# Optimization experiments

Measured on AMD Instinct MI355X. Metric: run time of the kernel, lower is better.

## Reference

```python
import jax, jax.numpy as jnp
import numpy as np

LN_EPS = 1e-5

def _layernorm(x, scale, bias):
    mu = jnp.mean(x, axis=-1, keepdims=True)
    var = jnp.var(x, axis=-1, keepdims=True)
    return (x - mu) * jax.lax.rsqrt(var + LN_EPS) * scale + bias

def setup_inputs() -> dict:
    T, node_num, num_nodes, E, C = 4, 10000, 50000, 256, 128
    key = jax.random.key(0)
    ks = jax.random.split(key, 12)
    s = lambda fan_in: 1.0 / np.sqrt(fan_in)
    return {
        "x": jax.random.normal(ks[0], (T * node_num, E), jnp.float32),
        "batched_x": jax.random.normal(ks[1], (num_nodes, E), jnp.float32),
        "indices": jax.random.randint(ks[2], (T, node_num), 0, num_nodes, jnp.int32),
        "ln_d_scale": jnp.ones((E,), jnp.float32),
        "ln_d_bias": jnp.zeros((E,), jnp.float32),
        "W1_d": jax.random.normal(ks[3], (E, 2 * E), jnp.float32) * s(E),
        "b1_d": jnp.zeros((2 * E,), jnp.float32),
        "W2_d": jax.random.normal(ks[4], (2 * E, C), jnp.float32) * s(2 * E),
        "b2_d": jnp.zeros((C,), jnp.float32),
        "ln_u_scale": jnp.ones((C,), jnp.float32),
        "ln_u_bias": jnp.zeros((C,), jnp.float32),
        "W1_u": jax.random.normal(ks[5], (C, 2 * C), jnp.float32) * s(C),
        "b1_u": jnp.zeros((2 * C,), jnp.float32),
        "W2_u": jax.random.normal(ks[6], (2 * C, E), jnp.float32) * s(2 * C),
        "b2_u": jnp.zeros((E,), jnp.float32),
    }

def reference(x, batched_x, indices, ln_d_scale, ln_d_bias, W1_d, b1_d, W2_d, b2_d,
              ln_u_scale, ln_u_bias, W1_u, b1_u, W2_u, b2_u):
    T, node_num = indices.shape
    num_nodes, E = batched_x.shape
    xr = x.reshape(T, node_num, E)
    # _to_entire: per-step scatter-add of active-node embeddings into the full node table
    def scatter_one(xi, idx):
        return jnp.zeros((num_nodes, E), x.dtype).at[idx].add(xi)
    ta = jax.vmap(scatter_one)(xr, indices)          # [T, num_nodes, E]
    inp = ta + batched_x[None]                        # broadcast entire features
    h = _layernorm(inp, ln_d_scale, ln_d_bias)
    h = jax.nn.gelu(h @ W1_d + b1_d, approximate=False) @ W2_d + b2_d  # [T, num_nodes, C]
    # _from_entire: gather each step's active nodes back, concat, LN + MLP up
    g = jnp.take_along_axis(h, indices[..., None], axis=1)  # [T, node_num, C]
    g = g.reshape(T * node_num, -1)
    g = _layernorm(g, ln_u_scale, ln_u_bias)
    out = jax.nn.gelu(g @ W1_u + b1_u, approximate=False) @ W2_u + b2_u  # [T*node_num, E]
    return out
```

## Files before the change

kernel.cpp:

```cpp
#include <hip/hip_runtime.h>
#include <math.h>

#define T_STEPS   4
#define NODE_NUM  10000
#define NUM_NODES 50000
#define E         256
#define TWO_E     512
#define CC        128
#define TWO_C     256
#define ROWS      32

typedef short bf16x8 __attribute__((ext_vector_type(8)));
typedef float f32x4  __attribute__((ext_vector_type(4)));

#define MFMA16(a, b, c) __builtin_amdgcn_mfma_f32_16x16x32_bf16((a), (b), (c), 0, 0, 0)

static __device__ unsigned short g_wt[294912];
static __device__ int g_cnt[T_STEPS * NUM_NODES];

__device__ __forceinline__ float geluf(float v) {
    return 0.5f * v * (1.0f + erff(v * 0.70710678118654752440f));
}

__device__ __forceinline__ unsigned short f2bf(float f) {
    unsigned int u = __builtin_bit_cast(unsigned int, f);
    u += 0x7fffu + ((u >> 16) & 1u);
    return (unsigned short)(u >> 16);
}

__global__ void prep_weights(const float* __restrict__ W1d, const float* __restrict__ W2d,
                             const float* __restrict__ W1u, const float* __restrict__ W2u) {
    int i = blockIdx.x * 256 + threadIdx.x;
    if (i < T_STEPS * NUM_NODES) g_cnt[i] = 0;
    if (i < 131072) {
        int n = i >> 8, k = i & 255;
        g_wt[i] = f2bf(W1d[(size_t)k * TWO_E + n]);
    }
    if (i < 65536) {
        int n = i >> 9, k = i & 511;
        g_wt[131072 + i] = f2bf(W2d[(size_t)k * CC + n]);
    }
    if (i < 32768) {
        int n = i >> 7, k = i & 127;
        g_wt[196608 + i] = f2bf(W1u[(size_t)k * TWO_C + n]);
    }
    if (i < 65536) {
        int n = i >> 8, k = i & 255;
        g_wt[229376 + i] = f2bf(W2u[(size_t)k * E + n]);
    }
}

__global__ void count_kernel(const int* __restrict__ indices) {
    int gr = blockIdx.x * 256 + threadIdx.x;
    if (gr < T_STEPS * NODE_NUM) {
        int t = gr / NODE_NUM;
        atomicAdd(&g_cnt[t * NUM_NODES + indices[gr]], 1);
    }
}

__global__ void zero_dup_kernel(float* __restrict__ table,
                                const int* __restrict__ indices,
                                int gr0, int t0) {
    int gr = gr0 + blockIdx.x * 4 + (threadIdx.x >> 6);
    int t = gr / NODE_NUM;
    int idx = indices[gr];
    if (g_cnt[t * NUM_NODES + idx] < 2) return;
    int c = (threadIdx.x & 63) * 4;
    float4 z = make_float4(0.f, 0.f, 0.f, 0.f);
    *reinterpret_cast<float4*>(&table[((size_t)(t - t0) * NUM_NODES + idx) * E + c]) = z;
}

__global__ void scatter_dup_kernel(float* __restrict__ table,
                                   const float* __restrict__ x,
                                   const int* __restrict__ indices,
                                   int gr0, int t0) {
    int gr = gr0 + blockIdx.x;
    int t = gr / NODE_NUM;
    int idx = indices[gr];
    if (g_cnt[t * NUM_NODES + idx] < 2) return;
    atomicAdd(&table[((size_t)(t - t0) * NUM_NODES + idx) * E + threadIdx.x],
              x[(size_t)gr * E + threadIdx.x]);
}

__global__ __launch_bounds__(256, 3)
void mlp_kernel(const float* __restrict__ table,
                const float* __restrict__ x,
                const float* __restrict__ batched_x,
                const int* __restrict__ indices,
                const float* __restrict__ lnd_s, const float* __restrict__ lnd_b,
                const float* __restrict__ b1d, const float* __restrict__ b2d,
                const float* __restrict__ lnu_s, const float* __restrict__ lnu_b,
                const float* __restrict__ b1u, const float* __restrict__ b2u,
                float* __restrict__ out,
                int gr0, int t0, int grLim) {
    __shared__ __align__(16) unsigned char smem[50176];
    __shared__ const float* rptr[ROWS];
    __shared__ int    ridx[ROWS];

    float*          Xf  = (float*)smem;
    unsigned short* Xs  = (unsigned short*)(smem + 33280);
    unsigned short* H1  = (unsigned short*)smem;
    float*          H2f = (float*)(smem + 33280);
    unsigned short* H2b = (unsigned short*)smem;
    unsigned short* G1  = (unsigned short*)(smem + 8704);

    const unsigned short* w1t  = g_wt;
    const unsigned short* w2t  = g_wt + 131072;
    const unsigned short* w1ut = g_wt + 196608;
    const unsigned short* w2ut = g_wt + 229376;

    const int tid = threadIdx.x;
    const int w = tid >> 6, lane = tid & 63;
    const int l16 = lane & 15, quad = lane >> 4;
    const int grb = gr0 + blockIdx.x * ROWS;

    if (tid < ROWS) {
        int gr = grb + tid;
        if (gr >= grLim) gr = grLim - 1;
        int t = gr / NODE_NUM;
        int idx = indices[gr];
        ridx[tid] = idx;
        rptr[tid] = (g_cnt[t * NUM_NODES + idx] > 1)
            ? (table + ((size_t)(t - t0) * NUM_NODES + idx) * E)
            : (x + (size_t)gr * E);
    }
    __syncthreads();

    #pragma unroll
    for (int it = 0; it < 8; ++it) {
        int v = it * 256 + tid;
        int r = v >> 6;
        int c = (v & 63) * 4;
        float4 tv = *reinterpret_cast<const float4*>(rptr[r] + c);
        float4 bv = *reinterpret_cast<const float4*>(&batched_x[(size_t)ridx[r] * E + c]);
        float4 s; s.x = tv.x + bv.x; s.y = tv.y + bv.y; s.z = tv.z + bv.z; s.w = tv.w + bv.w;
        *reinterpret_cast<float4*>(&Xf[r * 260 + c]) = s;
    }
    __syncthreads();

    {
        int row = tid >> 3, l8 = tid & 7;
        float s = 0.f, sq = 0.f;
        #pragma unroll
        for (int k = 0; k < 32; ++k) {
            float v = Xf[row * 260 + k * 8 + l8];
            s += v; sq += v * v;
        }
        s  += __shfl_xor(s, 1);  s  += __shfl_xor(s, 2);  s  += __shfl_xor(s, 4);
        sq += __shfl_xor(sq, 1); sq += __shfl_xor(sq, 2); sq += __shfl_xor(sq, 4);
        float mu = s * (1.0f / E);
        float var = sq * (1.0f / E) - mu * mu;
        float rs = rsqrtf(var + 1e-5f);
        #pragma unroll
        for (int k = 0; k < 32; ++k) {
            int c = k * 8 + l8;
            float v = (Xf[row * 260 + c] - mu) * rs * lnd_s[c] + lnd_b[c];
            Xs[row * 264 + c] = f2bf(v);
        }
    }
    __syncthreads();

    {
        bf16x8 af[2][8];
        #pragma unroll
        for (int mt = 0; mt < 2; ++mt) {
            const unsigned short* base = Xs + (l16 + 16 * mt) * 264 + quad * 8;
            #pragma unroll
            for (int ks = 0; ks < 8; ++ks)
                af[mt][ks] = *reinterpret_cast<const bf16x8*>(base + ks * 32);
        }
        #pragma unroll
        for (int nt_ = 0; nt_ < 8; ++nt_) {
            int n = (w * 8 + nt_) * 16 + l16;
            const unsigned short* bp = w1t + (size_t)n * 256 + quad * 8;
            f32x4 a0 = {0.f, 0.f, 0.f, 0.f}, a1 = {0.f, 0.f, 0.f, 0.f};
            #pragma unroll
            for (int ks = 0; ks < 8; ++ks) {
                bf16x8 b = *reinterpret_cast<const bf16x8*>(bp + ks * 32);
                a0 = MFMA16(af[0][ks], b, a0);
                a1 = MFMA16(af[1][ks], b, a1);
            }
            float bias = b1d[n];
            #pragma unroll
            for (int reg = 0; reg < 4; ++reg) {
                int r = quad * 4 + reg;
                H1[r * 520 + n]        = f2bf(geluf(a0[reg] + bias));
                H1[(r + 16) * 520 + n] = f2bf(geluf(a1[reg] + bias));
            }
        }
    }
    __syncthreads();

    {
        f32x4 acc2[2][2];
        #pragma unroll
        for (int i = 0; i < 2; ++i)
            #pragma unroll
            for (int j = 0; j < 2; ++j) acc2[i][j] = (f32x4){0.f, 0.f, 0.f, 0.f};
        #pragma unroll
        for (int kh = 0; kh < 2; ++kh) {
            bf16x8 af2[2][8];
            #pragma unroll
            for (int mt = 0; mt < 2; ++mt) {
                const unsigned short* base = H1 + (l16 + 16 * mt) * 520 + kh * 256 + quad * 8;
                #pragma unroll
                for (int ks = 0; ks < 8; ++ks)
                    af2[mt][ks] = *reinterpret_cast<const bf16x8*>(base + ks * 32);
            }
            #pragma unroll
            for (int nt2 = 0; nt2 < 2; ++nt2) {
                int n = (w * 2 + nt2) * 16 + l16;
                const unsigned short* bp = w2t + (size_t)n * 512 + kh * 256 + quad * 8;
                #pragma unroll
                for (int ks = 0; ks < 8; ++ks) {
                    bf16x8 b = *reinterpret_cast<const bf16x8*>(bp + ks * 32);
                    acc2[nt2][0] = MFMA16(af2[0][ks], b, acc2[nt2][0]);
                    acc2[nt2][1] = MFMA16(af2[1][ks], b, acc2[nt2][1]);
                }
            }
        }
        #pragma unroll
        for (int nt2 = 0; nt2 < 2; ++nt2) {
            int n = (w * 2 + nt2) * 16 + l16;
            float bias = b2d[n];
            #pragma unroll
            for (int mt = 0; mt < 2; ++mt)
                #pragma unroll
                for (int reg = 0; reg < 4; ++reg) {
                    int r = mt * 16 + quad * 4 + reg;
                    H2f[r * 132 + n] = acc2[nt2][mt][reg] + bias;
                }
        }
    }
    __syncthreads();

    {
        int row = tid >> 3, l8 = tid & 7;
        float s = 0.f, sq = 0.f;
        #pragma unroll
        for (int k = 0; k < 16; ++k) {
            float v = H2f[row * 132 + k * 8 + l8];
            s += v; sq += v * v;
        }
        s  += __shfl_xor(s, 1);  s  += __shfl_xor(s, 2);  s  += __shfl_xor(s, 4);
        sq += __shfl_xor(sq, 1); sq += __shfl_xor(sq, 2); sq += __shfl_xor(sq, 4);
        float mu = s * (1.0f / CC);
        float var = sq * (1.0f / CC) - mu * mu;
        float rs = rsqrtf(var + 1e-5f);
        #pragma unroll
        for (int k = 0; k < 16; ++k) {
            int c = k * 8 + l8;
            float v = (H2f[row * 132 + c] - mu) * rs * lnu_s[c] + lnu_b[c];
            H2b[row * 136 + c] = f2bf(v);
        }
    }
    __syncthreads();

    {
        bf16x8 af3[2][4];
        #pragma unroll
        for (int mt = 0; mt < 2; ++mt) {
            const unsigned short* base = H2b + (l16 + 16 * mt) * 136 + quad * 8;
            #pragma unroll
            for (int ks = 0; ks < 4; ++ks)
                af3[mt][ks] = *reinterpret_cast<const bf16x8*>(base + ks * 32);
        }
        #pragma unroll
        for (int nt_ = 0; nt_ < 4; ++nt_) {
            int n = (w * 4 + nt_) * 16 + l16;
            const unsigned short* bp = w1ut + (size_t)n * 128 + quad * 8;
            f32x4 a0 = {0.f, 0.f, 0.f, 0.f}, a1 = {0.f, 0.f, 0.f, 0.f};
            #pragma unroll
            for (int ks = 0; ks < 4; ++ks) {
                bf16x8 b = *reinterpret_cast<const bf16x8*>(bp + ks * 32);
                a0 = MFMA16(af3[0][ks], b, a0);
                a1 = MFMA16(af3[1][ks], b, a1);
            }
            float bias = b1u[n];
            #pragma unroll
            for (int reg = 0; reg < 4; ++reg) {
                int r = quad * 4 + reg;
                G1[r * 264 + n]        = f2bf(geluf(a0[reg] + bias));
                G1[(r + 16) * 264 + n] = f2bf(geluf(a1[reg] + bias));
            }
        }
    }
    __syncthreads();

    {
        bf16x8 af4[2][8];
        #pragma unroll
        for (int mt = 0; mt < 2; ++mt) {
            const unsigned short* base = G1 + (l16 + 16 * mt) * 264 + quad * 8;
            #pragma unroll
            for (int ks = 0; ks < 8; ++ks)
                af4[mt][ks] = *reinterpret_cast<const bf16x8*>(base + ks * 32);
        }
        #pragma unroll
        for (int nt_ = 0; nt_ < 4; ++nt_) {
            int n = (w * 4 + nt_) * 16 + l16;
            const unsigned short* bp = w2ut + (size_t)n * 256 + quad * 8;
            f32x4 a0 = {0.f, 0.f, 0.f, 0.f}, a1 = {0.f, 0.f, 0.f, 0.f};
            #pragma unroll
            for (int ks = 0; ks < 8; ++ks) {
                bf16x8 b = *reinterpret_cast<const bf16x8*>(bp + ks * 32);
                a0 = MFMA16(af4[0][ks], b, a0);
                a1 = MFMA16(af4[1][ks], b, a1);
            }
            float bias = b2u[n];
            #pragma unroll
            for (int reg = 0; reg < 4; ++reg) {
                int r = quad * 4 + reg;
                int g0 = grb + r, g1 = grb + r + 16;
                if (g0 < grLim) out[(size_t)g0 * E + n] = a0[reg] + bias;
                if (g1 < grLim) out[(size_t)g1 * E + n] = a1[reg] + bias;
            }
        }
    }
}

extern "C" void kernel_launch(void* const* d_in, const int* in_sizes, int n_in,
                              void* d_out, int out_size, void* d_ws, size_t ws_size,
                              hipStream_t stream) {
    const float* x     = (const float*)d_in[0];
    const float* bx    = (const float*)d_in[1];
    const int*   idxp  = (const int*)  d_in[2];
    const float* lnd_s = (const float*)d_in[3];
    const float* lnd_b = (const float*)d_in[4];
    const float* W1d   = (const float*)d_in[5];
    const float* b1d   = (const float*)d_in[6];
    const float* W2d   = (const float*)d_in[7];
    const float* b2d   = (const float*)d_in[8];
    const float* lnu_s = (const float*)d_in[9];
    const float* lnu_b = (const float*)d_in[10];
    const float* W1u   = (const float*)d_in[11];
    const float* b1u   = (const float*)d_in[12];
    const float* W2u   = (const float*)d_in[13];
    const float* b2u   = (const float*)d_in[14];
    float* out = (float*)d_out;
    float* table = (float*)d_ws;

    const size_t slice_bytes = (size_t)NUM_NODES * E * sizeof(float);
    int tb = (int)(ws_size / slice_bytes);
    if (tb < 1) tb = 1;
    if (tb > T_STEPS) tb = T_STEPS;

    prep_weights<<<784, 256, 0, stream>>>(W1d, W2d, W1u, W2u);
    count_kernel<<<(T_STEPS * NODE_NUM + 255) / 256, 256, 0, stream>>>(idxp);

    for (int t0 = 0; t0 < T_STEPS; t0 += tb) {
        int tcur = T_STEPS - t0 < tb ? T_STEPS - t0 : tb;
        int nrows = tcur * NODE_NUM;
        int gr0 = t0 * NODE_NUM;
        int grLim = gr0 + nrows;
        zero_dup_kernel   <<<nrows / 4, 256, 0, stream>>>(table, idxp, gr0, t0);
        scatter_dup_kernel<<<nrows, E, 0, stream>>>(table, x, idxp, gr0, t0);
        mlp_kernel<<<(nrows + ROWS - 1) / ROWS, 256, 0, stream>>>(
            table, x, bx, idxp, lnd_s, lnd_b, b1d, b2d,
            lnu_s, lnu_b, b1u, b2u, out, gr0, t0, grLim);
    }
}
```

Before: 293.0 us.

## Compact duplicate rows and shrink MLP shared memory for higher occupancy

The duplicate-row scatter is rebuilt around a compacted list. A compaction kernel zeroes each duplicate's table row and appends its index with an atomic counter, and a grid-stride kernel then scatters only the listed rows instead of launching one block per row. In the MLP kernel, the fp32 staging buffer in LDS is removed: rows are loaded straight into registers for the layernorm, and the buffers are aliased more tightly with extra barriers, cutting LDS from about 50KB to 33KB and raising launch bounds to 4 blocks per CU. The costs are higher register pressure, extra syncs, and atomic-ordering nondeterminism in the duplicate list.

```diff
diff --git a/kernel.cpp b/kernel.cpp
--- a/kernel.cpp
+++ b/kernel.cpp
@@ -12,11 +12,14 @@
 
 typedef short bf16x8 __attribute__((ext_vector_type(8)));
 typedef float f32x4  __attribute__((ext_vector_type(4)));
+typedef unsigned short u16x4 __attribute__((ext_vector_type(4)));
 
 #define MFMA16(a, b, c) __builtin_amdgcn_mfma_f32_16x16x32_bf16((a), (b), (c), 0, 0, 0)
 
 static __device__ unsigned short g_wt[294912];
 static __device__ int g_cnt[T_STEPS * NUM_NODES];
+static __device__ int g_dup[T_STEPS * NODE_NUM];
+static __device__ int g_ndup[T_STEPS];
 
 __device__ __forceinline__ float geluf(float v) {
     return 0.5f * v * (1.0f + erff(v * 0.70710678118654752440f));
@@ -32,6 +35,7 @@
                              const float* __restrict__ W1u, const float* __restrict__ W2u) {
     int i = blockIdx.x * 256 + threadIdx.x;
     if (i < T_STEPS * NUM_NODES) g_cnt[i] = 0;
+    if (i < T_STEPS) g_ndup[i] = 0;
     if (i < 131072) {
         int n = i >> 8, k = i & 255;
         g_wt[i] = f2bf(W1d[(size_t)k * TWO_E + n]);
@@ -58,31 +62,37 @@
     }
 }
 
-__global__ void zero_dup_kernel(float* __restrict__ table,
-                                const int* __restrict__ indices,
-                                int gr0, int t0) {
-    int gr = gr0 + blockIdx.x * 4 + (threadIdx.x >> 6);
+__global__ void compact_zero_kernel(float* __restrict__ table,
+                                    const int* __restrict__ indices,
+                                    int gr0, int t0, int grLim, int slab) {
+    int gr = gr0 + blockIdx.x * 256 + threadIdx.x;
+    if (gr >= grLim) return;
     int t = gr / NODE_NUM;
     int idx = indices[gr];
     if (g_cnt[t * NUM_NODES + idx] < 2) return;
-    int c = (threadIdx.x & 63) * 4;
+    int pos = atomicAdd(&g_ndup[slab], 1);
+    g_dup[gr0 + pos] = gr;
+    float4* rp = reinterpret_cast<float4*>(&table[((size_t)(t - t0) * NUM_NODES + idx) * E]);
     float4 z = make_float4(0.f, 0.f, 0.f, 0.f);
-    *reinterpret_cast<float4*>(&table[((size_t)(t - t0) * NUM_NODES + idx) * E + c]) = z;
-}
-
-__global__ void scatter_dup_kernel(float* __restrict__ table,
-                                   const float* __restrict__ x,
-                                   const int* __restrict__ indices,
-                                   int gr0, int t0) {
-    int gr = gr0 + blockIdx.x;
-    int t = gr / NODE_NUM;
-    int idx = indices[gr];
-    if (g_cnt[t * NUM_NODES + idx] < 2) return;
-    atomicAdd(&table[((size_t)(t - t0) * NUM_NODES + idx) * E + threadIdx.x],
-              x[(size_t)gr * E + threadIdx.x]);
-}
-
-__global__ __launch_bounds__(256, 3)
+    #pragma unroll
+    for (int k = 0; k < 64; ++k) rp[k] = z;
+}
+
+__global__ void scatter_list_kernel(float* __restrict__ table,
+                                    const float* __restrict__ x,
+                                    const int* __restrict__ indices,
+                                    int gr0, int t0, int slab) {
+    int nd = g_ndup[slab];
+    for (int e = blockIdx.x; e < nd; e += gridDim.x) {
+        int gr = g_dup[gr0 + e];
+        int t = gr / NODE_NUM;
+        int idx = indices[gr];
+        atomicAdd(&table[((size_t)(t - t0) * NUM_NODES + idx) * E + threadIdx.x],
+                  x[(size_t)gr * E + threadIdx.x]);
+    }
+}
+
+__global__ __launch_bounds__(256, 4)
 void mlp_kernel(const float* __restrict__ table,
                 const float* __restrict__ x,
                 const float* __restrict__ batched_x,
@@ -93,16 +103,13 @@
                 const float* __restrict__ b1u, const float* __restrict__ b2u,
                 float* __restrict__ out,
                 int gr0, int t0, int grLim) {
-    __shared__ __align__(16) unsigned char smem[50176];
-    __shared__ const float* rptr[ROWS];
-    __shared__ int    ridx[ROWS];
-
-    float*          Xf  = (float*)smem;
-    unsigned short* Xs  = (unsigned short*)(smem + 33280);
+    __shared__ __align__(16) unsigned char smem[33280];
+
+    unsigned short* Xs  = (unsigned short*)smem;
     unsigned short* H1  = (unsigned short*)smem;
-    float*          H2f = (float*)(smem + 33280);
-    unsigned short* H2b = (unsigned short*)smem;
-    unsigned short* G1  = (unsigned short*)(smem + 8704);
+    float*          H2f = (float*)smem;
+    unsigned short* H2b = (unsigned short*)(smem + 16896);
+    unsigned short* G1  = (unsigned short*)smem;
 
     const unsigned short* w1t  = g_wt;
     const unsigned short* w2t  = g_wt + 131072;
@@ -114,48 +121,44 @@
     const int l16 = lane & 15, quad = lane >> 4;
     const int grb = gr0 + blockIdx.x * ROWS;
 
-    if (tid < ROWS) {
-        int gr = grb + tid;
+    {
+        const int row = tid >> 3, l8 = tid & 7;
+        int gr = grb + row;
         if (gr >= grLim) gr = grLim - 1;
-        int t = gr / NODE_NUM;
-        int idx = indices[gr];
-        ridx[tid] = idx;
-        rptr[tid] = (g_cnt[t * NUM_NODES + idx] > 1)
+        const int t = gr / NODE_NUM;
+        const int idx = indices[gr];
+        const float* src = (g_cnt[t * NUM_NODES + idx] > 1)
             ? (table + ((size_t)(t - t0) * NUM_NODES + idx) * E)
             : (x + (size_t)gr * E);
-    }
-    __syncthreads();
-
-    #pragma unroll
-    for (int it = 0; it < 8; ++it) {
-        int v = it * 256 + tid;
-        int r = v >> 6;
-        int c = (v & 63) * 4;
-        float4 tv = *reinterpret_cast<const float4*>(rptr[r] + c);
-        float4 bv = *reinterpret_cast<const float4*>(&batched_x[(size_t)ridx[r] * E + c]);
-        float4 s; s.x = tv.x + bv.x; s.y = tv.y + bv.y; s.z = tv.z + bv.z; s.w = tv.w + bv.w;
-        *reinterpret_cast<float4*>(&Xf[r * 260 + c]) = s;
-    }
-    __syncthreads();
-
-    {
-        int row = tid >> 3, l8 = tid & 7;
+        const float* bxp = batched_x + (size_t)idx * E;
+        float v[32];
         float s = 0.f, sq = 0.f;
         #pragma unroll
-        for (int k = 0; k < 32; ++k) {
-            float v = Xf[row * 260 + k * 8 + l8];
-            s += v; sq += v * v;
+        for (int k = 0; k < 8; ++k) {
+            const int c = k * 32 + l8 * 4;
+            float4 a = *reinterpret_cast<const float4*>(src + c);
+            float4 b = *reinterpret_cast<const float4*>(bxp + c);
+            float4 u;
+            u.x = a.x + b.x; u.y = a.y + b.y; u.z = a.z + b.z; u.w = a.w + b.w;
+            v[k*4+0] = u.x; v[k*4+1] = u.y; v[k*4+2] = u.z; v[k*4+3] = u.w;
+            s  += u.x + u.y + u.z + u.w;
+            sq += u.x*u.x + u.y*u.y + u.z*u.z + u.w*u.w;
         }
         s  += __shfl_xor(s, 1);  s  += __shfl_xor(s, 2);  s  += __shfl_xor(s, 4);
         sq += __shfl_xor(sq, 1); sq += __shfl_xor(sq, 2); sq += __shfl_xor(sq, 4);
-        float mu = s * (1.0f / E);
-        float var = sq * (1.0f / E) - mu * mu;
-        float rs = rsqrtf(var + 1e-5f);
-        #pragma unroll
-        for (int k = 0; k < 32; ++k) {
-            int c = k * 8 + l8;
-            float v = (Xf[row * 260 + c] - mu) * rs * lnd_s[c] + lnd_b[c];
-            Xs[row * 264 + c] = f2bf(v);
+        const float mu = s * (1.0f / E);
+        const float rs = rsqrtf(sq * (1.0f / E) - mu * mu + 1e-5f);
+        #pragma unroll
+        for (int k = 0; k < 8; ++k) {
+            const int c = k * 32 + l8 * 4;
+            float4 sc = *reinterpret_cast<const float4*>(lnd_s + c);
+            float4 bi = *reinterpret_cast<const float4*>(lnd_b + c);
+            u16x4 o;
+            o.x = f2bf((v[k*4+0] - mu) * rs * sc.x + bi.x);
+            o.y = f2bf((v[k*4+1] - mu) * rs * sc.y + bi.y);
+            o.z = f2bf((v[k*4+2] - mu) * rs * sc.z + bi.z);
+            o.w = f2bf((v[k*4+3] - mu) * rs * sc.w + bi.w);
+            *reinterpret_cast<u16x4*>(&Xs[row * 264 + c]) = o;
         }
     }
     __syncthreads();
@@ -169,6 +172,7 @@
             for (int ks = 0; ks < 8; ++ks)
                 af[mt][ks] = *reinterpret_cast<const bf16x8*>(base + ks * 32);
         }
+        __syncthreads();
         #pragma unroll
         for (int nt_ = 0; nt_ < 8; ++nt_) {
             int n = (w * 8 + nt_) * 16 + l16;
@@ -197,26 +201,42 @@
         for (int i = 0; i < 2; ++i)
             #pragma unroll
             for (int j = 0; j < 2; ++j) acc2[i][j] = (f32x4){0.f, 0.f, 0.f, 0.f};
-        #pragma unroll
-        for (int kh = 0; kh < 2; ++kh) {
-            bf16x8 af2[2][8];
-            #pragma unroll
-            for (int mt = 0; mt < 2; ++mt) {
-                const unsigned short* base = H1 + (l16 + 16 * mt) * 520 + kh * 256 + quad * 8;
-                #pragma unroll
-                for (int ks = 0; ks < 8; ++ks)
-                    af2[mt][ks] = *reinterpret_cast<const bf16x8*>(base + ks * 32);
-            }
-            #pragma unroll
-            for (int nt2 = 0; nt2 < 2; ++nt2) {
-                int n = (w * 2 + nt2) * 16 + l16;
-                const unsigned short* bp = w2t + (size_t)n * 512 + kh * 256 + quad * 8;
-                #pragma unroll
-                for (int ks = 0; ks < 8; ++ks) {
-                    bf16x8 b = *reinterpret_cast<const bf16x8*>(bp + ks * 32);
-                    acc2[nt2][0] = MFMA16(af2[0][ks], b, acc2[nt2][0]);
-                    acc2[nt2][1] = MFMA16(af2[1][ks], b, acc2[nt2][1]);
-                }
+        bf16x8 af2[2][8];
+        #pragma unroll
+        for (int mt = 0; mt < 2; ++mt) {
+            const unsigned short* base = H1 + (l16 + 16 * mt) * 520 + quad * 8;
+            #pragma unroll
+            for (int ks = 0; ks < 8; ++ks)
+                af2[mt][ks] = *reinterpret_cast<const bf16x8*>(base + ks * 32);
+        }
+        #pragma unroll
+        for (int nt2 = 0; nt2 < 2; ++nt2) {
+            int n = (w * 2 + nt2) * 16 + l16;
+            const unsigned short* bp = w2t + (size_t)n * 512 + quad * 8;
+            #pragma unroll
+            for (int ks = 0; ks < 8; ++ks) {
+                bf16x8 b = *reinterpret_cast<const bf16x8*>(bp + ks * 32);
+                acc2[nt2][0] = MFMA16(af2[0][ks], b, acc2[nt2][0]);
+                acc2[nt2][1] = MFMA16(af2[1][ks], b, acc2[nt2][1]);
+            }
+        }
+        #pragma unroll
+        for (int mt = 0; mt < 2; ++mt) {
+            const unsigned short* base = H1 + (l16 + 16 * mt) * 520 + 256 + quad * 8;
+            #pragma unroll
+            for (int ks = 0; ks < 8; ++ks)
+                af2[mt][ks] = *reinterpret_cast<const bf16x8*>(base + ks * 32);
+        }
+        __syncthreads();
+        #pragma unroll
+        for (int nt2 = 0; nt2 < 2; ++nt2) {
+            int n = (w * 2 + nt2) * 16 + l16;
+            const unsigned short* bp = w2t + (size_t)n * 512 + 256 + quad * 8;
+            #pragma unroll
+            for (int ks = 0; ks < 8; ++ks) {
+                bf16x8 b = *reinterpret_cast<const bf16x8*>(bp + ks * 32);
+                acc2[nt2][0] = MFMA16(af2[0][ks], b, acc2[nt2][0]);
+                acc2[nt2][1] = MFMA16(af2[1][ks], b, acc2[nt2][1]);
             }
         }
         #pragma unroll
@@ -353,8 +373,10 @@
         int nrows = tcur * NODE_NUM;
         int gr0 = t0 * NODE_NUM;
         int grLim = gr0 + nrows;
-        zero_dup_kernel   <<<nrows / 4, 256, 0, stream>>>(table, idxp, gr0, t0);
-        scatter_dup_kernel<<<nrows, E, 0, stream>>>(table, x, idxp, gr0, t0);
+        int slab = t0 / tb;
+        compact_zero_kernel<<<(nrows + 255) / 256, 256, 0, stream>>>(
+            table, idxp, gr0, t0, grLim, slab);
+        scatter_list_kernel<<<1024, E, 0, stream>>>(table, x, idxp, gr0, t0, slab);
         mlp_kernel<<<(nrows + ROWS - 1) / ROWS, 256, 0, stream>>>(
             table, x, bx, idxp, lnd_s, lnd_b, b1d, b2d,
             lnu_s, lnu_b, b1u, b2u, out, gr0, t0, grLim);
```

Result: faster. 281.7 us (-3.9%).
